# Optimization experiments

Hardware: AMD Instinct MI355X
Metric: run time of the kernel (lower is better)

Reference implementation:

```python
import jax, jax.numpy as jnp
import numpy as np
from jax import lax

SEQ_LEN, BC, NODES, FEAT, HID, NUM_LAYER = 12, 16, 1024, 32, 64, 2
NEG_BIG = -1e16


def _gru_layer(x_seq, w_ih, w_hh, b_ih, b_hh):
    # x_seq: [T, B, in]; PyTorch gate order r, z, n
    B = x_seq.shape[1]
    h0 = jnp.zeros((B, w_hh.shape[1]), dtype=x_seq.dtype)

    def step(h, x):
        gi = x @ w_ih.T + b_ih
        gh = h @ w_hh.T + b_hh
        ir, iz, inn = jnp.split(gi, 3, axis=-1)
        hr, hz, hn = jnp.split(gh, 3, axis=-1)
        r = jax.nn.sigmoid(ir + hr)
        zg = jax.nn.sigmoid(iz + hz)
        n = jnp.tanh(inn + r * hn)
        h_new = (1.0 - zg) * n + zg * h
        return h_new, h_new

    h_T, ys = lax.scan(step, h0, x_seq)
    return ys, h_T


def _gat_aggregate(z_, maskf):
    # z_: [bc, nodes, H]; inner-product attention with leaky_relu(0.1) and adjacency mask
    att = jnp.einsum('bnd,bmd->bnm', z_, z_)
    att = jax.nn.leaky_relu(att, negative_slope=0.1) * maskf[None]
    att = jnp.where(att == 0.0, NEG_BIG, att)  # masked_fill_(atten==0, -1e16)
    att = jax.nn.softmax(att, axis=2)
    return jnp.einsum('bnm,bmd->bnd', att, z_)


def setup_inputs() -> dict:
    key = jax.random.key(0)
    ks = jax.random.split(key, 12)
    s = 1.0 / np.sqrt(HID)
    inp = {
        'h': jax.random.normal(ks[0], (SEQ_LEN, BC, NODES, FEAT), dtype=jnp.float32),
        'mask': jax.random.randint(ks[1], (NODES, NODES), 0, 2, dtype=jnp.int32),
        'w_ih0': jax.random.uniform(ks[2], (3 * HID, FEAT), minval=-s, maxval=s),
        'w_hh0': jax.random.uniform(ks[3], (3 * HID, HID), minval=-s, maxval=s),
        'b_ih0': jax.random.uniform(ks[4], (3 * HID,), minval=-s, maxval=s),
        'b_hh0': jax.random.uniform(ks[5], (3 * HID,), minval=-s, maxval=s),
        'w_ih1': jax.random.uniform(ks[6], (3 * HID, HID), minval=-s, maxval=s),
        'w_hh1': jax.random.uniform(ks[7], (3 * HID, HID), minval=-s, maxval=s),
        'b_ih1': jax.random.uniform(ks[8], (3 * HID,), minval=-s, maxval=s),
        'b_hh1': jax.random.uniform(ks[9], (3 * HID,), minval=-s, maxval=s),
    }
    return inp


def reference(h, mask, w_ih0, w_hh0, b_ih0, b_hh0, w_ih1, w_hh1, b_ih1, b_hh1):
    x = h.reshape(SEQ_LEN, BC * NODES, FEAT)
    ys0, hT0 = _gru_layer(x, w_ih0, w_hh0, b_ih0, b_hh0)
    _, hT1 = _gru_layer(ys0, w_ih1, w_hh1, b_ih1, b_hh1)
    # z: [num_layer, bc, nodes, H]
    z = jnp.stack([hT0, hT1]).reshape(NUM_LAYER, BC, NODES, HID)
    maskf = mask.astype(z.dtype)
    h_agg = jax.vmap(_gat_aggregate, in_axes=(0, None))(z, maskf)
    return h_agg  # [num_layer, bc, nodes, H]
```

## Files before the change

### kernel.cpp

```cpp
#include <hip/hip_runtime.h>
#include <math.h>

#define SEQ 12
#define NBATCH 16384
#define FEAT 32
#define HID 64
#define NSPLIT 4

#define WP_IH0 0
#define WP_HH0 6144
#define WP_IH1 18432
#define WP_HH1 30720
#define WP_TOTAL 43008

typedef __attribute__((ext_vector_type(8))) short bf16x8;
typedef __attribute__((ext_vector_type(4))) float f32x4;

#define MFMA_B16(A,B,C) __builtin_amdgcn_mfma_f32_16x16x32_bf16((A),(B),(C),0,0,0)

union B8u { unsigned short s[8]; bf16x8 v; };

__device__ __forceinline__ float sigf(float x) { return 1.0f / (1.0f + __expf(-x)); }
__device__ __forceinline__ float tanh_fast(float x) { return 2.0f / (1.0f + __expf(-2.0f * x)) - 1.0f; }

__device__ __forceinline__ unsigned int packsplit(float v) {
  unsigned int u  = __float_as_uint(v);
  unsigned int hi = u & 0xFFFF0000u;
  unsigned int lo = __float_as_uint(v - __uint_as_float(hi)) >> 16;
  return hi | lo;
}

__device__ __forceinline__ void unpack8(const unsigned int* p, bf16x8& H, bf16x8& L) {
  uint4 u0 = *(const uint4*)p;
  uint4 u1 = *(const uint4*)(p + 4);
  unsigned int uu[8] = {u0.x, u0.y, u0.z, u0.w, u1.x, u1.y, u1.z, u1.w};
  B8u hh, ll;
  #pragma unroll
  for (int i = 0; i < 8; i++) {
    hh.s[i] = (unsigned short)(uu[i] >> 16);
    ll.s[i] = (unsigned short)(uu[i] & 0xFFFFu);
  }
  H = hh.v; L = ll.v;
}

__device__ __forceinline__ void split8(const float* fa, bf16x8& H, bf16x8& L) {
  B8u hh, ll;
  #pragma unroll
  for (int i = 0; i < 8; i++) {
    unsigned int u  = __float_as_uint(fa[i]);
    unsigned int hi = u & 0xFFFF0000u;
    hh.s[i] = (unsigned short)(hi >> 16);
    ll.s[i] = (unsigned short)(__float_as_uint(fa[i] - __uint_as_float(hi)) >> 16);
  }
  H = hh.v; L = ll.v;
}

#define DOT4(acc, A_, B_)                                   \
  acc = fmaf((A_).x, (B_).x, acc);                          \
  acc = fmaf((A_).y, (B_).y, acc);                          \
  acc = fmaf((A_).z, (B_).z, acc);                          \
  acc = fmaf((A_).w, (B_).w, acc);

__global__ void prep_frag_kernel(const float* __restrict__ w_ih0, const float* __restrict__ w_hh0,
                                 const float* __restrict__ w_ih1, const float* __restrict__ w_hh1,
                                 unsigned short* __restrict__ wf)
{
  int i = blockIdx.x * blockDim.x + threadIdx.x;
  if (i >= 43008) return;
  const float* src; int K, rel, baseS;
  if (i < 6144)       { src = w_ih0; K = 32; rel = i;         baseS = 0; }
  else if (i < 18432) { src = w_hh0; K = 64; rel = i - 6144;  baseS = 12288; }
  else if (i < 30720) { src = w_ih1; K = 64; rel = i - 18432; baseS = 36864; }
  else                { src = w_hh1; K = 64; rel = i - 30720; baseS = 61440; }
  int nks = K / 32;
  int fp   = rel >> 9;
  int lane = (rel >> 3) & 63;
  int e    = rel & 7;
  int ct = fp / nks, ks = fp % nks;
  int g = ct * 16 + (lane & 15);
  int k = ks * 32 + (lane >> 4) * 8 + e;
  float v = src[g * K + k];
  unsigned int u = __float_as_uint(v);
  unsigned short hi = (unsigned short)(u >> 16);
  float hif = __uint_as_float(u & 0xFFFF0000u);
  unsigned short lo = (unsigned short)(__float_as_uint(v - hif) >> 16);
  int out = baseS + fp * 1024 + lane * 8 + e;
  wf[out]       = hi;
  wf[out + 512] = lo;
}

__global__ void mask_pack(const int* __restrict__ mask, unsigned int* __restrict__ mbits)
{
  int i = blockIdx.x * blockDim.x + threadIdx.x;
  if (i >= 32768) return;
  int r = i >> 5, wd = i & 31;
  const int* mp = mask + (size_t)r * 1024 + wd * 32;
  unsigned int b = 0;
  #pragma unroll
  for (int k = 0; k < 32; k++) b |= (mp[k] != 0 ? 1u : 0u) << k;
  mbits[i] = b;
}

__global__ __launch_bounds__(256, 2) void gru_fused(
    const float* __restrict__ x, const unsigned short* __restrict__ wf,
    const float* __restrict__ b_ih0, const float* __restrict__ b_hh0,
    const float* __restrict__ b_ih1, const float* __restrict__ b_hh1,
    unsigned int* __restrict__ zpk0, unsigned int* __restrict__ zpk1)
{
  __shared__ unsigned int h0l[2][16 * 68];
  __shared__ unsigned int h1l[2][16 * 68];
  const int tid = threadIdx.x;
  const int w = tid >> 6, l = tid & 63, lr = l & 15, lg = l >> 4;
  const int s0 = blockIdx.x * 16;
  const int j = w * 16 + lr;

  bf16x8 Wih0[3][2], Whh0[3][2][2], Wih1[3][2][2], Whh1[3][2][2];
  #pragma unroll
  for (int g = 0; g < 3; g++) {
    const int ct = w + g * 4;
    Wih0[g][0] = *(const bf16x8*)&wf[ct * 1024 + l * 8];
    Wih0[g][1] = *(const bf16x8*)&wf[ct * 1024 + 512 + l * 8];
    #pragma unroll
    for (int ks = 0; ks < 2; ks++) {
      Whh0[g][ks][0] = *(const bf16x8*)&wf[12288 + (ct * 2 + ks) * 1024 + l * 8];
      Whh0[g][ks][1] = *(const bf16x8*)&wf[12288 + (ct * 2 + ks) * 1024 + 512 + l * 8];
      Wih1[g][ks][0] = *(const bf16x8*)&wf[36864 + (ct * 2 + ks) * 1024 + l * 8];
      Wih1[g][ks][1] = *(const bf16x8*)&wf[36864 + (ct * 2 + ks) * 1024 + 512 + l * 8];
      Whh1[g][ks][0] = *(const bf16x8*)&wf[61440 + (ct * 2 + ks) * 1024 + l * 8];
      Whh1[g][ks][1] = *(const bf16x8*)&wf[61440 + (ct * 2 + ks) * 1024 + 512 + l * 8];
    }
  }

  const float br0  = b_ih0[j]      + b_hh0[j];
  const float bz0  = b_ih0[64 + j] + b_hh0[64 + j];
  const float bni0 = b_ih0[128 + j];
  const float bnh0 = b_hh0[128 + j];
  const float br1  = b_ih1[j]      + b_hh1[j];
  const float bz1  = b_ih1[64 + j] + b_hh1[64 + j];
  const float bni1 = b_ih1[128 + j];
  const float bnh1 = b_hh1[128 + j];

  for (int i = tid; i < 1088; i += 256) { h0l[0][i] = 0u; h1l[0][i] = 0u; }
  float hD0[4] = {0.f, 0.f, 0.f, 0.f};
  float hD1[4] = {0.f, 0.f, 0.f, 0.f};
  __syncthreads();

  float4 xc0 = *(const float4*)(x + ((size_t)s0 + lr) * FEAT + lg * 8);
  float4 xc1 = *(const float4*)(x + ((size_t)s0 + lr) * FEAT + lg * 8 + 4);

  int pb = 0;
  #pragma unroll 1
  for (int t = 0; t < SEQ; t++) {
    const int cb = pb ^ 1;
    float4 xn0, xn1;
    if (t < SEQ - 1) {
      const float* xp = x + ((size_t)(t + 1) * NBATCH + s0 + lr) * FEAT + lg * 8;
      xn0 = *(const float4*)xp;
      xn1 = *(const float4*)(xp + 4);
    }

    f32x4 aR, aZ, aNI, aNH;
    #pragma unroll
    for (int e = 0; e < 4; e++) { aR[e] = br0; aZ[e] = bz0; aNI[e] = bni0; aNH[e] = bnh0; }
    {
      float fa[8] = {xc0.x, xc0.y, xc0.z, xc0.w, xc1.x, xc1.y, xc1.z, xc1.w};
      bf16x8 Ah, Al;
      split8(fa, Ah, Al);
      aR  = MFMA_B16(Ah, Wih0[0][0], aR);  aR  = MFMA_B16(Al, Wih0[0][0], aR);  aR  = MFMA_B16(Ah, Wih0[0][1], aR);
      aZ  = MFMA_B16(Ah, Wih0[1][0], aZ);  aZ  = MFMA_B16(Al, Wih0[1][0], aZ);  aZ  = MFMA_B16(Ah, Wih0[1][1], aZ);
      aNI = MFMA_B16(Ah, Wih0[2][0], aNI); aNI = MFMA_B16(Al, Wih0[2][0], aNI); aNI = MFMA_B16(Ah, Wih0[2][1], aNI);
    }
    #pragma unroll
    for (int ks = 0; ks < 2; ks++) {
      bf16x8 Ah, Al;
      unpack8(&h0l[pb][lr * 68 + ks * 32 + lg * 8], Ah, Al);
      aR  = MFMA_B16(Ah, Whh0[0][ks][0], aR);  aR  = MFMA_B16(Al, Whh0[0][ks][0], aR);  aR  = MFMA_B16(Ah, Whh0[0][ks][1], aR);
      aZ  = MFMA_B16(Ah, Whh0[1][ks][0], aZ);  aZ  = MFMA_B16(Al, Whh0[1][ks][0], aZ);  aZ  = MFMA_B16(Ah, Whh0[1][ks][1], aZ);
      aNH = MFMA_B16(Ah, Whh0[2][ks][0], aNH); aNH = MFMA_B16(Al, Whh0[2][ks][0], aNH); aNH = MFMA_B16(Ah, Whh0[2][ks][1], aNH);
    }
    #pragma unroll
    for (int e = 0; e < 4; e++) {
      float rg = sigf(aR[e]);
      float zg = sigf(aZ[e]);
      float n  = tanh_fast(fmaf(rg, aNH[e], aNI[e]));
      float hn = fmaf(zg, hD0[e] - n, n);
      hD0[e] = hn;
      h0l[cb][(lg * 4 + e) * 68 + j] = packsplit(hn);
    }
    __syncthreads();

    #pragma unroll
    for (int e = 0; e < 4; e++) { aR[e] = br1; aZ[e] = bz1; aNI[e] = bni1; aNH[e] = bnh1; }
    #pragma unroll
    for (int ks = 0; ks < 2; ks++) {
      bf16x8 Ah, Al;
      unpack8(&h0l[cb][lr * 68 + ks * 32 + lg * 8], Ah, Al);
      aR  = MFMA_B16(Ah, Wih1[0][ks][0], aR);  aR  = MFMA_B16(Al, Wih1[0][ks][0], aR);  aR  = MFMA_B16(Ah, Wih1[0][ks][1], aR);
      aZ  = MFMA_B16(Ah, Wih1[1][ks][0], aZ);  aZ  = MFMA_B16(Al, Wih1[1][ks][0], aZ);  aZ  = MFMA_B16(Ah, Wih1[1][ks][1], aZ);
      aNI = MFMA_B16(Ah, Wih1[2][ks][0], aNI); aNI = MFMA_B16(Al, Wih1[2][ks][0], aNI); aNI = MFMA_B16(Ah, Wih1[2][ks][1], aNI);
    }
    #pragma unroll
    for (int ks = 0; ks < 2; ks++) {
      bf16x8 Ah, Al;
      unpack8(&h1l[pb][lr * 68 + ks * 32 + lg * 8], Ah, Al);
      aR  = MFMA_B16(Ah, Whh1[0][ks][0], aR);  aR  = MFMA_B16(Al, Whh1[0][ks][0], aR);  aR  = MFMA_B16(Ah, Whh1[0][ks][1], aR);
      aZ  = MFMA_B16(Ah, Whh1[1][ks][0], aZ);  aZ  = MFMA_B16(Al, Whh1[1][ks][0], aZ);  aZ  = MFMA_B16(Ah, Whh1[1][ks][1], aZ);
      aNH = MFMA_B16(Ah, Whh1[2][ks][0], aNH); aNH = MFMA_B16(Al, Whh1[2][ks][0], aNH); aNH = MFMA_B16(Ah, Whh1[2][ks][1], aNH);
    }
    #pragma unroll
    for (int e = 0; e < 4; e++) {
      float rg = sigf(aR[e]);
      float zg = sigf(aZ[e]);
      float n  = tanh_fast(fmaf(rg, aNH[e], aNI[e]));
      float hn = fmaf(zg, hD1[e] - n, n);
      hD1[e] = hn;
      h1l[cb][(lg * 4 + e) * 68 + j] = packsplit(hn);
    }
    if (t == SEQ - 1) {
      #pragma unroll
      for (int e = 0; e < 4; e++) {
        int sl = lg * 4 + e;
        zpk0[(size_t)(s0 + sl) * 64 + j] = packsplit(hD0[e]);
        zpk1[(size_t)(s0 + sl) * 64 + j] = packsplit(hD1[e]);
      }
    }
    __syncthreads();
    xc0 = xn0; xc1 = xn1;
    pb = cb;
  }
}

__global__ void prep_kernel(const float* __restrict__ w_ih0, const float* __restrict__ w_hh0,
                            const float* __restrict__ w_ih1, const float* __restrict__ w_hh1,
                            float* __restrict__ wp)
{
  for (int i = blockIdx.x * blockDim.x + threadIdx.x; i < WP_TOTAL; i += gridDim.x * blockDim.x) {
    const float* src;
    int K, rel;
    if (i < WP_HH0)      { src = w_ih0; K = 32; rel = i; }
    else if (i < WP_IH1) { src = w_hh0; K = 64; rel = i - WP_HH0; }
    else if (i < WP_HH1) { src = w_ih1; K = 64; rel = i - WP_IH1; }
    else                 { src = w_hh1; K = 64; rel = i - WP_HH1; }
    int kr = rel & 3;
    int jj = (rel >> 2) & 63;
    int rest = rel >> 8;
    int g = rest % 3;
    int k4 = rest / 3;
    wp[i] = src[(g * 64 + jj) * K + k4 * 4 + kr];
  }
}

__global__ __launch_bounds__(256, 1) void gru_fallback(
    const float* __restrict__ x, const float* __restrict__ wpack,
    const float* __restrict__ b_ih0, const float* __restrict__ b_hh0,
    const float* __restrict__ b_ih1, const float* __restrict__ b_hh1,
    unsigned int* __restrict__ zout)
{
  __shared__ float wlds[36864];
  __shared__ float h0s[16][64];
  __shared__ float h1s[16][64];
  const int tid = threadIdx.x;
  {
    const float4* src = (const float4*)(wpack + WP_HH0);
    float4* dst = (float4*)wlds;
    #pragma unroll 4
    for (int i = tid; i < 9216; i += 256) dst[i] = src[i];
  }
  const int j  = tid & 63;
  const int sg = __builtin_amdgcn_readfirstlane(tid >> 6);
  const float br0  = b_ih0[j]      + b_hh0[j];
  const float bz0  = b_ih0[64 + j] + b_hh0[64 + j];
  const float bni0 = b_ih0[128 + j];
  const float bnh0 = b_hh0[128 + j];
  const float br1  = b_ih1[j]      + b_hh1[j];
  const float bz1  = b_ih1[64 + j] + b_hh1[64 + j];
  const float bni1 = b_ih1[128 + j];
  const float bnh1 = b_hh1[128 + j];
  const int s0 = blockIdx.x * 16;
  float h0r[4] = {0.f, 0.f, 0.f, 0.f};
  float h1r[4] = {0.f, 0.f, 0.f, 0.f};
  #pragma unroll
  for (int ss = 0; ss < 4; ss++) { h0s[sg * 4 + ss][j] = 0.f; h1s[sg * 4 + ss][j] = 0.f; }
  __syncthreads();
  const float4* wih0g = (const float4*)(wpack + WP_IH0);
  const float4* whh0l = (const float4*)(wlds);
  const float4* wih1l = (const float4*)(wlds + 12288);
  const float4* whh1l = (const float4*)(wlds + 24576);
  for (int t = 0; t < SEQ; t++) {
    float ar[4], az[4], ani[4], anh[4];
    #pragma unroll
    for (int ss = 0; ss < 4; ss++) { ar[ss] = br0; az[ss] = bz0; ani[ss] = bni0; anh[ss] = bnh0; }
    const float4* xr0 = (const float4*)(x + ((size_t)t * NBATCH + (s0 + sg * 4 + 0)) * FEAT);
    const float4* xr1 = (const float4*)(x + ((size_t)t * NBATCH + (s0 + sg * 4 + 1)) * FEAT);
    const float4* xr2 = (const float4*)(x + ((size_t)t * NBATCH + (s0 + sg * 4 + 2)) * FEAT);
    const float4* xr3 = (const float4*)(x + ((size_t)t * NBATCH + (s0 + sg * 4 + 3)) * FEAT);
    #pragma unroll
    for (int k4 = 0; k4 < 8; k4++) {
      float4 wr = wih0g[(k4 * 3 + 0) * 64 + j];
      float4 wz = wih0g[(k4 * 3 + 1) * 64 + j];
      float4 wn = wih0g[(k4 * 3 + 2) * 64 + j];
      float4 xv[4] = {xr0[k4], xr1[k4], xr2[k4], xr3[k4]};
      #pragma unroll
      for (int ss = 0; ss < 4; ss++) {
        DOT4(ar[ss],  wr, xv[ss]);
        DOT4(az[ss],  wz, xv[ss]);
        DOT4(ani[ss], wn, xv[ss]);
      }
    }
    #pragma unroll
    for (int k4 = 0; k4 < 16; k4++) {
      float4 wr = whh0l[(k4 * 3 + 0) * 64 + j];
      float4 wz = whh0l[(k4 * 3 + 1) * 64 + j];
      float4 wn = whh0l[(k4 * 3 + 2) * 64 + j];
      #pragma unroll
      for (int ss = 0; ss < 4; ss++) {
        float4 hv = *(const float4*)&h0s[sg * 4 + ss][k4 * 4];
        DOT4(ar[ss],  wr, hv);
        DOT4(az[ss],  wz, hv);
        DOT4(anh[ss], wn, hv);
      }
    }
    float h0n[4];
    #pragma unroll
    for (int ss = 0; ss < 4; ss++) {
      float rg = sigf(ar[ss]);
      float zg = sigf(az[ss]);
      float ng = tanh_fast(fmaf(rg, anh[ss], ani[ss]));
      h0n[ss] = fmaf(zg, h0r[ss] - ng, ng);
    }
    __syncthreads();
    #pragma unroll
    for (int ss = 0; ss < 4; ss++) { h0s[sg * 4 + ss][j] = h0n[ss]; h0r[ss] = h0n[ss]; }
    __syncthreads();
    #pragma unroll
    for (int ss = 0; ss < 4; ss++) { ar[ss] = br1; az[ss] = bz1; ani[ss] = bni1; anh[ss] = bnh1; }
    #pragma unroll
    for (int k4 = 0; k4 < 16; k4++) {
      float4 wr = wih1l[(k4 * 3 + 0) * 64 + j];
      float4 wz = wih1l[(k4 * 3 + 1) * 64 + j];
      float4 wn = wih1l[(k4 * 3 + 2) * 64 + j];
      #pragma unroll
      for (int ss = 0; ss < 4; ss++) {
        float4 hv = *(const float4*)&h0s[sg * 4 + ss][k4 * 4];
        DOT4(ar[ss],  wr, hv);
        DOT4(az[ss],  wz, hv);
        DOT4(ani[ss], wn, hv);
      }
    }
    #pragma unroll
    for (int k4 = 0; k4 < 16; k4++) {
      float4 wr = whh1l[(k4 * 3 + 0) * 64 + j];
      float4 wz = whh1l[(k4 * 3 + 1) * 64 + j];
      float4 wn = whh1l[(k4 * 3 + 2) * 64 + j];
      #pragma unroll
      for (int ss = 0; ss < 4; ss++) {
        float4 hv = *(const float4*)&h1s[sg * 4 + ss][k4 * 4];
        DOT4(ar[ss],  wr, hv);
        DOT4(az[ss],  wz, hv);
        DOT4(anh[ss], wn, hv);
      }
    }
    float h1n[4];
    #pragma unroll
    for (int ss = 0; ss < 4; ss++) {
      float rg = sigf(ar[ss]);
      float zg = sigf(az[ss]);
      float ng = tanh_fast(fmaf(rg, anh[ss], ani[ss]));
      h1n[ss] = fmaf(zg, h1r[ss] - ng, ng);
    }
    __syncthreads();
    #pragma unroll
    for (int ss = 0; ss < 4; ss++) { h1s[sg * 4 + ss][j] = h1n[ss]; h1r[ss] = h1n[ss]; }
    __syncthreads();
  }
  #pragma unroll
  for (int ss = 0; ss < 4; ss++) {
    int s = s0 + sg * 4 + ss;
    zout[(size_t)s * 64 + j]            = packsplit(h0r[ss]);
    zout[(size_t)(NBATCH + s) * 64 + j] = packsplit(h1r[ss]);
  }
}

__global__ __launch_bounds__(256, 4) void gat_mfma4(
    const unsigned int* __restrict__ zpk, const unsigned int* __restrict__ mbits,
    float* __restrict__ partO, float* __restrict__ partD,
    float* __restrict__ out, int nsplit)
{
  __shared__ unsigned int VT[64 * 68];
  __shared__ float        PS[64 * 68];
  const int tid = threadIdx.x;
  const int w = tid >> 6, l = tid & 63, lr = l & 15, lg = l >> 4;
  const int blk  = blockIdx.x;
  const int lbrt = blk / nsplit;
  const int half = blk - lbrt * nsplit;
  const int rt = lbrt & 15;
  const int lb = lbrt >> 4;
  const int tiles = 16 / nsplit;
  const int mt0 = half * tiles;
  const unsigned int* zb = zpk + (size_t)lb * 65536;
  const int n0 = rt * 64;

  bf16x8 Qh[2], Ql[2];
  #pragma unroll
  for (int ks = 0; ks < 2; ks++)
    unpack8(&zb[(size_t)(n0 + w * 16 + lr) * 64 + ks * 32 + lg * 8], Qh[ks], Ql[ks]);

  f32x4 O[4];
  float D[4] = {0.f, 0.f, 0.f, 0.f};
  #pragma unroll
  for (int ct = 0; ct < 4; ct++)
    #pragma unroll
    for (int e = 0; e < 4; e++) O[ct][e] = 0.f;

  #pragma unroll 1
  for (int mt = mt0; mt < mt0 + tiles; ++mt) {
    __syncthreads();
    {
      unsigned int tmp[16];
      #pragma unroll
      for (int r = 0; r < 16; r++)
        tmp[r] = zb[(size_t)(mt * 64 + w * 16 + r) * 64 + l];
      #pragma unroll
      for (int q = 0; q < 4; q++)
        *(uint4*)&VT[l * 68 + w * 16 + q * 4] =
            make_uint4(tmp[q * 4], tmp[q * 4 + 1], tmp[q * 4 + 2], tmp[q * 4 + 3]);
    }
    __syncthreads();

    f32x4 S[4];
    #pragma unroll
    for (int ct = 0; ct < 4; ct++)
      #pragma unroll
      for (int e = 0; e < 4; e++) S[ct][e] = 0.f;
    #pragma unroll
    for (int ks = 0; ks < 2; ks++) {
      #pragma unroll
      for (int ct = 0; ct < 4; ct++) {
        bf16x8 Kh, Kl;
        unpack8(&zb[(size_t)(mt * 64 + ct * 16 + lr) * 64 + ks * 32 + lg * 8], Kh, Kl);
        S[ct] = MFMA_B16(Qh[ks], Kh, S[ct]);
        S[ct] = MFMA_B16(Ql[ks], Kh, S[ct]);
        S[ct] = MFMA_B16(Qh[ks], Kl, S[ct]);
      }
    }

    #pragma unroll
    for (int e = 0; e < 4; e++) {
      const int row = n0 + w * 16 + lg * 4 + e;
      const uint2 mw = *(const uint2*)&mbits[(size_t)row * 32 + mt * 2];
      const unsigned int sel[4] = {mw.x >> lr, mw.x >> (16 + lr), mw.y >> lr, mw.y >> (16 + lr)};
      float ds = 0.f;
      #pragma unroll
      for (int ct = 0; ct < 4; ct++) {
        float v = S[ct][e];
        float lrv = v > 0.f ? v : 0.1f * v;
        float p = ((sel[ct] & 1u) && lrv != 0.0f) ? __expf(lrv - 64.0f) : 0.0f;
        ds += p;
        PS[(w * 16 + lg * 4 + e) * 68 + ct * 16 + lr] = p;
      }
      D[e] += ds;
    }

    #pragma unroll
    for (int ks = 0; ks < 2; ks++) {
      const float* pp = &PS[(w * 16 + lr) * 68 + ks * 32 + lg * 8];
      float4 p0 = *(const float4*)pp;
      float4 p1 = *(const float4*)(pp + 4);
      float fa[8] = {p0.x, p0.y, p0.z, p0.w, p1.x, p1.y, p1.z, p1.w};
      B8u H;
      #pragma unroll
      for (int i = 0; i < 8; i++)
        H.s[i] = (unsigned short)((__float_as_uint(fa[i]) + 0x8000u) >> 16);
      bf16x8 Ph = H.v;
      #pragma unroll
      for (int ct = 0; ct < 4; ct++) {
        bf16x8 Vh, Vl;
        unpack8(&VT[(ct * 16 + lr) * 68 + ks * 32 + lg * 8], Vh, Vl);
        O[ct] = MFMA_B16(Ph, Vh, O[ct]);
        O[ct] = MFMA_B16(Ph, Vl, O[ct]);
      }
    }
  }

  #pragma unroll
  for (int e = 0; e < 4; e++) {
    #pragma unroll
    for (int sw = 1; sw < 16; sw <<= 1) D[e] += __shfl_xor(D[e], sw, 16);
  }

  if (nsplit == 1) {
    #pragma unroll
    for (int e = 0; e < 4; e++) {
      float inv = 1.0f / D[e];
      size_t rowo = ((size_t)lb * 1024 + n0 + w * 16 + lg * 4 + e) * 64;
      #pragma unroll
      for (int ct = 0; ct < 4; ct++)
        out[rowo + ct * 16 + lr] = O[ct][e] * inv;
    }
  } else {
    float* po = partO + (size_t)blk * 4096;
    #pragma unroll
    for (int e = 0; e < 4; e++) {
      int row = w * 16 + lg * 4 + e;
      #pragma unroll
      for (int ct = 0; ct < 4; ct++)
        po[row * 64 + ct * 16 + lr] = O[ct][e];
      if (lr == 0) partD[(size_t)blk * 64 + row] = D[e];
    }
  }
}

__global__ __launch_bounds__(256) void gat_combine(
    const float* __restrict__ partO, const float* __restrict__ partD,
    float* __restrict__ out, int nsplit)
{
  const int lbrt = blockIdx.x;
  const int q  = threadIdx.x >> 2;
  const int dc = (threadIdx.x & 3) * 16;
  float dt = 0.f;
  for (int i = 0; i < nsplit; i++) dt += partD[(size_t)(lbrt * nsplit + i) * 64 + q];
  float inv = 1.0f / dt;
  float* op = out + ((size_t)lbrt * 64 + q) * 64 + dc;
  #pragma unroll
  for (int v = 0; v < 4; v++) {
    float4 acc = make_float4(0.f, 0.f, 0.f, 0.f);
    for (int i = 0; i < nsplit; i++) {
      const float4 o = *(const float4*)(partO + (size_t)(lbrt * nsplit + i) * 4096 + q * 64 + dc + v * 4);
      acc.x += o.x; acc.y += o.y; acc.z += o.z; acc.w += o.w;
    }
    *(float4*)(op + v * 4) = make_float4(acc.x * inv, acc.y * inv, acc.z * inv, acc.w * inv);
  }
}

extern "C" void kernel_launch(void* const* d_in, const int* in_sizes, int n_in,
                              void* d_out, int out_size, void* d_ws, size_t ws_size,
                              hipStream_t stream) {
  const float* h     = (const float*)d_in[0];
  const int*   mask  = (const int*)d_in[1];
  const float* w_ih0 = (const float*)d_in[2];
  const float* w_hh0 = (const float*)d_in[3];
  const float* b_ih0 = (const float*)d_in[4];
  const float* b_hh0 = (const float*)d_in[5];
  const float* w_ih1 = (const float*)d_in[6];
  const float* w_hh1 = (const float*)d_in[7];
  const float* b_ih1 = (const float*)d_in[8];
  const float* b_hh1 = (const float*)d_in[9];
  float* out = (float*)d_out;

  char* wsb = (char*)d_ws;
  unsigned int* zpk = (unsigned int*)wsb;
  const size_t Z_BYTES  = (size_t)2 * NBATCH * 64 * 4;
  const size_t PART_OFF = Z_BYTES + 176128;
  const size_t PO_BYTES = (size_t)512 * NSPLIT * 4096 * 4;
  const size_t PD_BYTES = (size_t)512 * NSPLIT * 64 * 4;
  const size_t MB_OFF   = PART_OFF + PO_BYTES + PD_BYTES;
  const size_t NEED_FAST = MB_OFF + 131072;

  if (ws_size >= NEED_FAST) {
    unsigned short* wfrag = (unsigned short*)(wsb + Z_BYTES);
    float* partO  = (float*)(wsb + PART_OFF);
    float* partD  = (float*)(wsb + PART_OFF + PO_BYTES);
    unsigned int* mbits = (unsigned int*)(wsb + MB_OFF);
    prep_frag_kernel<<<168, 256, 0, stream>>>(w_ih0, w_hh0, w_ih1, w_hh1, wfrag);
    mask_pack<<<128, 256, 0, stream>>>(mask, mbits);
    gru_fused<<<1024, 256, 0, stream>>>(h, wfrag, b_ih0, b_hh0, b_ih1, b_hh1,
                                        zpk, zpk + (size_t)NBATCH * 64);
    gat_mfma4<<<512 * NSPLIT, 256, 0, stream>>>(zpk, mbits, partO, partD, out, NSPLIT);
    gat_combine<<<512, 256, 0, stream>>>(partO, partD, out, NSPLIT);
  } else {
    float* wpack = (float*)(wsb + Z_BYTES);
    unsigned int* mbits = (unsigned int*)(wsb + Z_BYTES + 172032);
    prep_kernel<<<24, 256, 0, stream>>>(w_ih0, w_hh0, w_ih1, w_hh1, wpack);
    mask_pack<<<128, 256, 0, stream>>>(mask, mbits);
    gru_fallback<<<1024, 256, 0, stream>>>(h, wpack, b_ih0, b_hh0, b_ih1, b_hh1, zpk);
    gat_mfma4<<<512, 256, 0, stream>>>(zpk, mbits, nullptr, nullptr, out, 1);
  }
}
```

Measured before the change: 180.5 us.

## Split hidden-state LDS into hi/lo arrays, drop per-step barrier, raise occupancy

Hidden states now live in separate bf16 hi and lo shared arrays with a padded stride, so MFMA A-fragments load directly as vectors instead of being unpacked from packed 32-bit words. The second __syncthreads per timestep is removed, relying on double buffering to keep reads and writes apart. The final state store moves out of the loop. Launch bounds go from 2 to 4 blocks per CU, which halves the per-thread register budget. With about 168 VGPRs of register-resident weights, that raises a real risk of spilling.

```diff
diff --git a/kernel.cpp b/kernel.cpp
--- a/kernel.cpp
+++ b/kernel.cpp
@@ -101,14 +101,15 @@
   mbits[i] = b;
 }
 
-__global__ __launch_bounds__(256, 2) void gru_fused(
+#define HSTR 72
+__global__ __launch_bounds__(256, 4) void gru_fused(
     const float* __restrict__ x, const unsigned short* __restrict__ wf,
     const float* __restrict__ b_ih0, const float* __restrict__ b_hh0,
     const float* __restrict__ b_ih1, const float* __restrict__ b_hh1,
     unsigned int* __restrict__ zpk0, unsigned int* __restrict__ zpk1)
 {
-  __shared__ unsigned int h0l[2][16 * 68];
-  __shared__ unsigned int h1l[2][16 * 68];
+  __shared__ unsigned short h0h[2][16 * HSTR], h0o[2][16 * HSTR];
+  __shared__ unsigned short h1h[2][16 * HSTR], h1o[2][16 * HSTR];
   const int tid = threadIdx.x;
   const int w = tid >> 6, l = tid & 63, lr = l & 15, lg = l >> 4;
   const int s0 = blockIdx.x * 16;
@@ -140,7 +141,9 @@
   const float bni1 = b_ih1[128 + j];
   const float bnh1 = b_hh1[128 + j];
 
-  for (int i = tid; i < 1088; i += 256) { h0l[0][i] = 0u; h1l[0][i] = 0u; }
+  for (int i = tid; i < 16 * HSTR; i += 256) {
+    h0h[0][i] = 0; h0o[0][i] = 0; h1h[0][i] = 0; h1o[0][i] = 0;
+  }
   float hD0[4] = {0.f, 0.f, 0.f, 0.f};
   float hD1[4] = {0.f, 0.f, 0.f, 0.f};
   __syncthreads();
@@ -172,8 +175,8 @@
     }
     #pragma unroll
     for (int ks = 0; ks < 2; ks++) {
-      bf16x8 Ah, Al;
-      unpack8(&h0l[pb][lr * 68 + ks * 32 + lg * 8], Ah, Al);
+      bf16x8 Ah = *(const bf16x8*)&h0h[pb][lr * HSTR + ks * 32 + lg * 8];
+      bf16x8 Al = *(const bf16x8*)&h0o[pb][lr * HSTR + ks * 32 + lg * 8];
       aR  = MFMA_B16(Ah, Whh0[0][ks][0], aR);  aR  = MFMA_B16(Al, Whh0[0][ks][0], aR);  aR  = MFMA_B16(Ah, Whh0[0][ks][1], aR);
       aZ  = MFMA_B16(Ah, Whh0[1][ks][0], aZ);  aZ  = MFMA_B16(Al, Whh0[1][ks][0], aZ);  aZ  = MFMA_B16(Ah, Whh0[1][ks][1], aZ);
       aNH = MFMA_B16(Ah, Whh0[2][ks][0], aNH); aNH = MFMA_B16(Al, Whh0[2][ks][0], aNH); aNH = MFMA_B16(Ah, Whh0[2][ks][1], aNH);
@@ -185,7 +188,10 @@
       float n  = tanh_fast(fmaf(rg, aNH[e], aNI[e]));
       float hn = fmaf(zg, hD0[e] - n, n);
       hD0[e] = hn;
-      h0l[cb][(lg * 4 + e) * 68 + j] = packsplit(hn);
+      unsigned int pk = packsplit(hn);
+      int idx = (lg * 4 + e) * HSTR + j;
+      h0h[cb][idx] = (unsigned short)(pk >> 16);
+      h0o[cb][idx] = (unsigned short)(pk & 0xFFFFu);
     }
     __syncthreads();
 
@@ -193,16 +199,16 @@
     for (int e = 0; e < 4; e++) { aR[e] = br1; aZ[e] = bz1; aNI[e] = bni1; aNH[e] = bnh1; }
     #pragma unroll
     for (int ks = 0; ks < 2; ks++) {
-      bf16x8 Ah, Al;
-      unpack8(&h0l[cb][lr * 68 + ks * 32 + lg * 8], Ah, Al);
+      bf16x8 Ah = *(const bf16x8*)&h0h[cb][lr * HSTR + ks * 32 + lg * 8];
+      bf16x8 Al = *(const bf16x8*)&h0o[cb][lr * HSTR + ks * 32 + lg * 8];
       aR  = MFMA_B16(Ah, Wih1[0][ks][0], aR);  aR  = MFMA_B16(Al, Wih1[0][ks][0], aR);  aR  = MFMA_B16(Ah, Wih1[0][ks][1], aR);
       aZ  = MFMA_B16(Ah, Wih1[1][ks][0], aZ);  aZ  = MFMA_B16(Al, Wih1[1][ks][0], aZ);  aZ  = MFMA_B16(Ah, Wih1[1][ks][1], aZ);
       aNI = MFMA_B16(Ah, Wih1[2][ks][0], aNI); aNI = MFMA_B16(Al, Wih1[2][ks][0], aNI); aNI = MFMA_B16(Ah, Wih1[2][ks][1], aNI);
     }
     #pragma unroll
     for (int ks = 0; ks < 2; ks++) {
-      bf16x8 Ah, Al;
-      unpack8(&h1l[pb][lr * 68 + ks * 32 + lg * 8], Ah, Al);
+      bf16x8 Ah = *(const bf16x8*)&h1h[pb][lr * HSTR + ks * 32 + lg * 8];
+      bf16x8 Al = *(const bf16x8*)&h1o[pb][lr * HSTR + ks * 32 + lg * 8];
       aR  = MFMA_B16(Ah, Whh1[0][ks][0], aR);  aR  = MFMA_B16(Al, Whh1[0][ks][0], aR);  aR  = MFMA_B16(Ah, Whh1[0][ks][1], aR);
       aZ  = MFMA_B16(Ah, Whh1[1][ks][0], aZ);  aZ  = MFMA_B16(Al, Whh1[1][ks][0], aZ);  aZ  = MFMA_B16(Ah, Whh1[1][ks][1], aZ);
       aNH = MFMA_B16(Ah, Whh1[2][ks][0], aNH); aNH = MFMA_B16(Al, Whh1[2][ks][0], aNH); aNH = MFMA_B16(Ah, Whh1[2][ks][1], aNH);
@@ -214,19 +220,20 @@
       float n  = tanh_fast(fmaf(rg, aNH[e], aNI[e]));
       float hn = fmaf(zg, hD1[e] - n, n);
       hD1[e] = hn;
-      h1l[cb][(lg * 4 + e) * 68 + j] = packsplit(hn);
-    }
-    if (t == SEQ - 1) {
-      #pragma unroll
-      for (int e = 0; e < 4; e++) {
-        int sl = lg * 4 + e;
-        zpk0[(size_t)(s0 + sl) * 64 + j] = packsplit(hD0[e]);
-        zpk1[(size_t)(s0 + sl) * 64 + j] = packsplit(hD1[e]);
-      }
-    }
-    __syncthreads();
+      unsigned int pk = packsplit(hn);
+      int idx = (lg * 4 + e) * HSTR + j;
+      h1h[cb][idx] = (unsigned short)(pk >> 16);
+      h1o[cb][idx] = (unsigned short)(pk & 0xFFFFu);
+    }
     xc0 = xn0; xc1 = xn1;
     pb = cb;
+  }
+
+  #pragma unroll
+  for (int e = 0; e < 4; e++) {
+    int sl = lg * 4 + e;
+    zpk0[(size_t)(s0 + sl) * 64 + j] = packsplit(hD0[e]);
+    zpk1[(size_t)(s0 + sl) * 64 + j] = packsplit(hD1[e]);
   }
 }
 
```

Measured after the change: 378.9 us. 2.1x slower.
